# Optimization experiments

Measured on AMD Instinct MI355X. Metric: run time of the kernel, lower is better.

The kernel has to match this reference:

```python
import jax, jax.numpy as jnp
import numpy as np

D_MODEL = 1024
NUM_HEAD = 16
D_HEAD = D_MODEL // NUM_HEAD
NEG_INF = -1e9


def setup_inputs() -> dict:
    key = jax.random.key(0)
    ks = jax.random.split(key, 10)
    B, S = 16, 512
    v = jax.random.normal(ks[0], (B, S, D_MODEL), dtype=jnp.float32)
    lengths = jax.random.randint(ks[1], (B,), 1, S + 1, dtype=jnp.int32)
    scale = 0.02
    Wq = jax.random.normal(ks[2], (D_MODEL, D_MODEL), dtype=jnp.float32) * scale
    bq = jnp.zeros((D_MODEL,), dtype=jnp.float32)
    Wk = jax.random.normal(ks[3], (D_MODEL, D_MODEL), dtype=jnp.float32) * scale
    bk = jnp.zeros((D_MODEL,), dtype=jnp.float32)
    Wv = jax.random.normal(ks[4], (D_MODEL, D_MODEL), dtype=jnp.float32) * scale
    bv = jnp.zeros((D_MODEL,), dtype=jnp.float32)
    Wo = jax.random.normal(ks[5], (D_MODEL, D_MODEL), dtype=jnp.float32) * scale
    bo = jnp.zeros((D_MODEL,), dtype=jnp.float32)
    return {"v": v, "lengths": lengths, "Wq": Wq, "bq": bq, "Wk": Wk,
            "bk": bk, "Wv": Wv, "bv": bv, "Wo": Wo, "bo": bo}


def reference(v, lengths, Wq, bq, Wk, bk, Wv, bv, Wo, bo):
    B, S, D = v.shape
    H, Dh = NUM_HEAD, D_HEAD
    # key-padding mask: True where key position j is valid (j < lengths[b])
    valid = jnp.arange(S)[None, :] < lengths[:, None]          # [B, S]
    # project q, k, v and split heads -> [B, H, S, Dh]
    def split_heads(x):
        return x.reshape(B, S, H, Dh).transpose(0, 2, 1, 3)
    q = split_heads(v @ Wq + bq)
    k = split_heads(v @ Wk + bk)
    val = split_heads(v @ Wv + bv)
    scores = jnp.einsum('bhqd,bhkd->bhqk', q, k) / jnp.sqrt(jnp.float32(Dh))
    scores = jnp.where(valid[:, None, None, :], scores, NEG_INF)  # mask padded keys
    attn = jax.nn.softmax(scores, axis=-1)
    out = jnp.einsum('bhqk,bhkd->bhqd', attn, val)              # [B, H, S, Dh]
    out = out.transpose(0, 2, 1, 3).reshape(B, S, D)
    return out @ Wo + bo
```

## Files before the change

### kernel.cpp

```cpp
#include <hip/hip_runtime.h>
#include <hip/hip_bf16.h>

typedef unsigned short u16;
typedef __attribute__((ext_vector_type(8))) short short8;
typedef __attribute__((ext_vector_type(4))) float f32x4;

#define B_SZ 16
#define S_SZ 512
#define D_SZ 1024
#define H_SZ 16
#define DH_SZ 64
#define M_SZ (B_SZ * S_SZ)
#define EXPSCALE 0.18033688f

__device__ __forceinline__ void gload_lds16(const void* g, void* l) {
  __builtin_amdgcn_global_load_lds(
      (const __attribute__((address_space(1))) unsigned int*)g,
      (__attribute__((address_space(3))) unsigned int*)l,
      16, 0, 0);
}

__global__ __launch_bounds__(256) void prep(
    const float* __restrict__ v, u16* __restrict__ vB,
    const float* __restrict__ W0, const float* __restrict__ W1,
    const float* __restrict__ W2, const float* __restrict__ W3,
    u16* __restrict__ T0, u16* __restrict__ T1,
    u16* __restrict__ T2, u16* __restrict__ T3) {
  __shared__ float tile[32][33];
  const int bid = blockIdx.x;
  if (bid < 8192) {
    int i = bid * 256 + threadIdx.x;
    const float4 f = *(const float4*)&v[(size_t)i * 4];
    ushort4 o; __hip_bfloat16 h;
    h = __float2bfloat16(f.x); o.x = *(u16*)&h;
    h = __float2bfloat16(f.y); o.y = *(u16*)&h;
    h = __float2bfloat16(f.z); o.z = *(u16*)&h;
    h = __float2bfloat16(f.w); o.w = *(u16*)&h;
    *(ushort4*)&vB[(size_t)i * 4] = o;
    return;
  }
  const int tb = bid - 8192;
  const int z = tb >> 10, rem = tb & 1023;
  const int by = rem >> 5, bx = rem & 31;
  const float* W; u16* T;
  switch (z) {
    case 0: W = W0; T = T0; break;
    case 1: W = W1; T = T1; break;
    case 2: W = W2; T = T2; break;
    default: W = W3; T = T3; break;
  }
  int tx = threadIdx.x & 31, ty = threadIdx.x >> 5;
  int x = bx * 32 + tx;
#pragma unroll
  for (int i = 0; i < 32; i += 8)
    tile[ty + i][tx] = W[(size_t)(by * 32 + ty + i) * 1024 + x];
  __syncthreads();
  int x2 = by * 32 + tx;
#pragma unroll
  for (int i = 0; i < 32; i += 8) {
    __hip_bfloat16 h = __float2bfloat16(tile[tx][ty + i]);
    T[(size_t)(bx * 32 + ty + i) * 1024 + x2] = *(u16*)&h;
  }
}

struct G8 {
  const u16* A; const u16* Bt;
  u16* As; u16* Bs;
  int m0, n0;
  int wave, c, quad, r7, wm, wn;
  int srow, slc8;
};

#define AS_T (128 * 64)
#define BS_T (256 * 64)

__device__ __forceinline__ void stage_a(const G8& g, int buf, int kt, int i) {
  const int grp = g.wave * 2 + i;
  gload_lds16(&g.A[(size_t)(g.m0 + grp * 8 + g.srow) * 1024 + kt * 64 + g.slc8],
              g.As + buf * AS_T + grp * 512);
}
__device__ __forceinline__ void stage_b(const G8& g, int buf, int kt, int i) {
  const int grp = g.wave * 4 + i;
  gload_lds16(&g.Bt[(size_t)(g.n0 + grp * 8 + g.srow) * 1024 + kt * 64 + g.slc8],
              g.Bs + buf * BS_T + grp * 512);
}

template<bool ST, int VM>
__device__ __forceinline__ void tile_step(const G8& g, int cur, int stg, int kt2,
                                          f32x4 acc[4][4]) {
  const u16* ab = g.As + cur * AS_T;
  const u16* bb = g.Bs + cur * BS_T;
  short8 af[4], bf[4];

  {
    const int pc = (g.quad ^ g.r7) * 8;
#pragma unroll
    for (int i = 0; i < 4; ++i) {
      af[i] = *(const short8*)&ab[(g.wm + i * 16 + g.c) * 64 + pc];
      bf[i] = *(const short8*)&bb[(g.wn + i * 16 + g.c) * 64 + pc];
    }
    if constexpr (ST) {
      stage_a(g, stg, kt2, 0);
      stage_a(g, stg, kt2, 1);
      stage_b(g, stg, kt2, 0);
    }
    __builtin_amdgcn_s_barrier();
    __builtin_amdgcn_s_setprio(1);
#pragma unroll
    for (int mi = 0; mi < 4; ++mi)
#pragma unroll
      for (int ni = 0; ni < 4; ++ni)
        acc[mi][ni] = __builtin_amdgcn_mfma_f32_16x16x32_bf16(
            af[mi], bf[ni], acc[mi][ni], 0, 0, 0);
    __builtin_amdgcn_s_setprio(0);
    __builtin_amdgcn_s_barrier();
  }

  {
    const int pc = ((4 + g.quad) ^ g.r7) * 8;
#pragma unroll
    for (int i = 0; i < 4; ++i) {
      af[i] = *(const short8*)&ab[(g.wm + i * 16 + g.c) * 64 + pc];
      bf[i] = *(const short8*)&bb[(g.wn + i * 16 + g.c) * 64 + pc];
    }
    if constexpr (ST) {
      stage_b(g, stg, kt2, 1);
      stage_b(g, stg, kt2, 2);
      stage_b(g, stg, kt2, 3);
    }
    __builtin_amdgcn_s_barrier();
    __builtin_amdgcn_s_setprio(1);
#pragma unroll
    for (int mi = 0; mi < 4; ++mi)
#pragma unroll
      for (int ni = 0; ni < 4; ++ni)
        acc[mi][ni] = __builtin_amdgcn_mfma_f32_16x16x32_bf16(
            af[mi], bf[ni], acc[mi][ni], 0, 0, 0);
    __builtin_amdgcn_s_setprio(0);
    if constexpr (VM == 6) {
      asm volatile("s_waitcnt vmcnt(6)" ::: "memory");
      __builtin_amdgcn_s_barrier();
    } else if constexpr (VM == 0) {
      asm volatile("s_waitcnt vmcnt(0)" ::: "memory");
      __builtin_amdgcn_s_barrier();
    }
  }
}

__device__ __forceinline__ void gemm_core8(
    const u16* __restrict__ A, const u16* __restrict__ Bt,
    u16* AsB, u16* BsB, int m0, int n0, f32x4 acc[4][4]) {
  const int tid = threadIdx.x;
  const int lane = tid & 63;
  G8 g;
  g.A = A; g.Bt = Bt; g.As = AsB; g.Bs = BsB;
  g.m0 = m0; g.n0 = n0;
  g.wave = tid >> 6;
  g.c = lane & 15; g.quad = lane >> 4; g.r7 = g.c & 7;
  g.wm = (g.wave >> 2) * 64;
  g.wn = (g.wave & 3) * 64;
  g.srow = lane >> 3;
  g.slc8 = ((lane & 7) ^ g.srow) * 8;

  stage_a(g, 0, 0, 0); stage_a(g, 0, 0, 1);
  stage_b(g, 0, 0, 0); stage_b(g, 0, 0, 1); stage_b(g, 0, 0, 2); stage_b(g, 0, 0, 3);
  stage_a(g, 1, 1, 0); stage_a(g, 1, 1, 1);
  stage_b(g, 1, 1, 0); stage_b(g, 1, 1, 1); stage_b(g, 1, 1, 2); stage_b(g, 1, 1, 3);
  asm volatile("s_waitcnt vmcnt(6)" ::: "memory");
  __builtin_amdgcn_s_barrier();

  int cur = 0, stg = 2;
#pragma unroll 1
  for (int t = 0; t < 14; ++t) {
    tile_step<true, 6>(g, cur, stg, t + 2, acc);
    cur = (cur == 2) ? 0 : cur + 1;
    stg = (stg == 2) ? 0 : stg + 1;
  }
  tile_step<false, 0>(g, cur, 0, 0, acc);
  tile_step<false, -1>(g, 0, 0, 0, acc);
}

template<int Z>
__global__ __launch_bounds__(512, 2) void gemm_split(
    const u16* __restrict__ A, const u16* __restrict__ Bt,
    const float* __restrict__ bias, u16* __restrict__ Out) {
  __shared__ u16 As[3][AS_T];
  __shared__ u16 Bs[3][BS_T];
  const int m0 = blockIdx.x * 128, n0 = blockIdx.y * 256;

  f32x4 acc[4][4];
#pragma unroll
  for (int i = 0; i < 4; ++i)
#pragma unroll
    for (int j = 0; j < 4; ++j) acc[i][j] = f32x4{0.f, 0.f, 0.f, 0.f};

  gemm_core8(A, Bt, &As[0][0], &Bs[0][0], m0, n0, acc);

  const int lane = threadIdx.x & 63, wave = threadIdx.x >> 6;
  const int wm = (wave >> 2) * 64, wn = (wave & 3) * 64;
  const int c = lane & 15, quad = lane >> 4;
#pragma unroll
  for (int ni = 0; ni < 4; ++ni) {
    int n = n0 + wn + ni * 16 + c;
    float bval = bias[n];
#pragma unroll
    for (int mi = 0; mi < 4; ++mi) {
      int mb = m0 + wm + mi * 16 + quad * 4;
      if constexpr (Z == 2) {
        int bb = mb >> 9, s = mb & 511, hh = n >> 6, d = n & 63;
        ushort4 st;
        __hip_bfloat16 h0 = __float2bfloat16(acc[mi][ni][0] + bval); st.x = *(u16*)&h0;
        __hip_bfloat16 h1 = __float2bfloat16(acc[mi][ni][1] + bval); st.y = *(u16*)&h1;
        __hip_bfloat16 h2 = __float2bfloat16(acc[mi][ni][2] + bval); st.z = *(u16*)&h2;
        __hip_bfloat16 h3 = __float2bfloat16(acc[mi][ni][3] + bval); st.w = *(u16*)&h3;
        *(ushort4*)&Out[(((size_t)(bb * 16 + hh) * 64 + d) << 9) + s] = st;
      } else {
#pragma unroll
        for (int r = 0; r < 4; ++r) {
          int m = mb + r;
          float val = acc[mi][ni][r] + bval;
          __hip_bfloat16 hb = __float2bfloat16(val);
          if constexpr (Z == 0) {
            Out[(size_t)m * 1024 + n] = *(u16*)&hb;
          } else {
            int bb = m >> 9, s = m & 511, hh = n >> 6, d = n & 63;
            Out[(((size_t)(bb * 16 + hh) * 512 + s) << 6) + d] = *(u16*)&hb;
          }
        }
      }
    }
  }
}

__global__ __launch_bounds__(512, 2) void gemm_out(
    const u16* __restrict__ A, const u16* __restrict__ Bt,
    const float* __restrict__ bias, float* __restrict__ Cf) {
  __shared__ u16 As[3][AS_T];
  __shared__ u16 Bs[3][BS_T];
  const int m0 = blockIdx.x * 128, n0 = blockIdx.y * 256;

  f32x4 acc[4][4];
#pragma unroll
  for (int i = 0; i < 4; ++i)
#pragma unroll
    for (int j = 0; j < 4; ++j) acc[i][j] = f32x4{0.f, 0.f, 0.f, 0.f};

  gemm_core8(A, Bt, &As[0][0], &Bs[0][0], m0, n0, acc);

  const int lane = threadIdx.x & 63, wave = threadIdx.x >> 6;
  const int wm = (wave >> 2) * 64, wn = (wave & 3) * 64;
  const int c = lane & 15, quad = lane >> 4;
#pragma unroll
  for (int ni = 0; ni < 4; ++ni) {
    int n = n0 + wn + ni * 16 + c;
    float bval = bias[n];
#pragma unroll
    for (int mi = 0; mi < 4; ++mi) {
#pragma unroll
      for (int r = 0; r < 4; ++r) {
        int m = m0 + wm + mi * 16 + quad * 4 + r;
        Cf[(size_t)m * 1024 + n] = acc[mi][ni][r] + bval;
      }
    }
  }
}

__global__ __launch_bounds__(256) void attn_v6(
    const u16* __restrict__ Q, const u16* __restrict__ Kt,
    const u16* __restrict__ Vt, const int* __restrict__ lengths,
    u16* __restrict__ O) {
  const int qc = blockIdx.x, h = blockIdx.y, b = blockIdx.z;
  const int t = threadIdx.x;
  const int lane = t & 63, wave = t >> 6;
  const int c = lane & 15, quad = lane >> 4;
  const int kb = quad * 8;
  const int len = lengths[b];
  const int q0 = qc * 128 + wave * 32;

  __shared__ __align__(16) u16 Ks[64 * 64];
  __shared__ __align__(16) u16 Vs[64 * 64];
  __shared__ __align__(16) u16 Pt[4][32 * 72];

  const size_t bBase = (size_t)b * (S_SZ * D_SZ);
  const size_t hBase = ((size_t)(b * H_SZ + h)) * (S_SZ * DH_SZ);

  short8 aq[2][2];
#pragma unroll
  for (int qt = 0; qt < 2; ++qt) {
    aq[qt][0] = *(const short8*)&Q[bBase + (size_t)(q0 + qt * 16 + c) * 1024 + h * 64 + kb];
    aq[qt][1] = *(const short8*)&Q[bBase + (size_t)(q0 + qt * 16 + c) * 1024 + h * 64 + 32 + kb];
  }

  const int srow = lane >> 3;
  const int slc = (lane & 7) ^ srow;

  float rs[2] = {0.f, 0.f};
  f32x4 o[2][4];
#pragma unroll
  for (int qt = 0; qt < 2; ++qt)
#pragma unroll
    for (int i = 0; i < 4; ++i) o[qt][i] = f32x4{0.f, 0.f, 0.f, 0.f};

  const int kmax = (len + 63) & ~63;
  for (int k0 = 0; k0 < kmax; k0 += 64) {
    __syncthreads();
#pragma unroll
    for (int g = 0; g < 2; ++g) {
      const int rb = (wave * 2 + g) * 8;
      gload_lds16(&Kt[hBase + (size_t)(k0 + rb + srow) * 64 + slc * 8],
                  &Ks[(wave * 2 + g) * 512]);
      gload_lds16(&Vt[hBase + (size_t)(rb + srow) * 512 + k0 + slc * 8],
                  &Vs[(wave * 2 + g) * 512]);
    }
    __syncthreads();

#pragma unroll
    for (int sub = 0; sub < 4; ++sub) {
      const int row = sub * 16 + c;
      short8 bk0 = *(const short8*)&Ks[row * 64 + ((quad ^ (c & 7))) * 8];
      short8 bk1 = *(const short8*)&Ks[row * 64 + (((4 + quad) ^ (c & 7))) * 8];
      const int keyb = k0 + sub * 16 + quad * 4;
#pragma unroll
      for (int qt = 0; qt < 2; ++qt) {
        f32x4 s = {0.f, 0.f, 0.f, 0.f};
        s = __builtin_amdgcn_mfma_f32_16x16x32_bf16(bk0, aq[qt][0], s, 0, 0, 0);
        s = __builtin_amdgcn_mfma_f32_16x16x32_bf16(bk1, aq[qt][1], s, 0, 0, 0);
        ushort4 st;
        float p0 = (keyb + 0) < len ? exp2f(s[0] * EXPSCALE) : 0.f;
        float p1 = (keyb + 1) < len ? exp2f(s[1] * EXPSCALE) : 0.f;
        float p2 = (keyb + 2) < len ? exp2f(s[2] * EXPSCALE) : 0.f;
        float p3 = (keyb + 3) < len ? exp2f(s[3] * EXPSCALE) : 0.f;
        __hip_bfloat16 h0 = __float2bfloat16(p0); st.x = *(u16*)&h0;
        __hip_bfloat16 h1 = __float2bfloat16(p1); st.y = *(u16*)&h1;
        __hip_bfloat16 h2 = __float2bfloat16(p2); st.z = *(u16*)&h2;
        __hip_bfloat16 h3 = __float2bfloat16(p3); st.w = *(u16*)&h3;
        rs[qt] += __bfloat162float(h0) + __bfloat162float(h1) +
                  __bfloat162float(h2) + __bfloat162float(h3);
        *(ushort4*)&Pt[wave][(qt * 16 + c) * 72 + sub * 16 + quad * 4] = st;
      }
    }
#pragma unroll
    for (int ksub = 0; ksub < 2; ++ksub) {
      const short8 pa0 = *(const short8*)&Pt[wave][(c) * 72 + ksub * 32 + kb];
      const short8 pa1 = *(const short8*)&Pt[wave][(16 + c) * 72 + ksub * 32 + kb];
#pragma unroll
      for (int dt = 0; dt < 4; ++dt) {
        const int vrow = dt * 16 + c;
        short8 vb = *(const short8*)&Vs[vrow * 64 + (((ksub * 4 + quad) ^ (c & 7))) * 8];
        o[0][dt] = __builtin_amdgcn_mfma_f32_16x16x32_bf16(pa0, vb, o[0][dt], 0, 0, 0);
        o[1][dt] = __builtin_amdgcn_mfma_f32_16x16x32_bf16(pa1, vb, o[1][dt], 0, 0, 0);
      }
    }
  }

#pragma unroll
  for (int qt = 0; qt < 2; ++qt) {
    rs[qt] += __shfl_xor(rs[qt], 16, 64);
    rs[qt] += __shfl_xor(rs[qt], 32, 64);
  }

#pragma unroll
  for (int qt = 0; qt < 2; ++qt) {
    float lq[4];
#pragma unroll
    for (int r = 0; r < 4; ++r) lq[r] = __shfl(rs[qt], quad * 4 + r, 16);
#pragma unroll
    for (int dt = 0; dt < 4; ++dt) {
#pragma unroll
      for (int r = 0; r < 4; ++r) {
        int s = q0 + qt * 16 + quad * 4 + r;
        float val = o[qt][dt][r] / lq[r];
        __hip_bfloat16 ob = __float2bfloat16(val);
        O[bBase + (size_t)s * 1024 + h * 64 + dt * 16 + c] = *(u16*)&ob;
      }
    }
  }
}

extern "C" void kernel_launch(void* const* d_in, const int* in_sizes, int n_in,
                              void* d_out, int out_size, void* d_ws, size_t ws_size,
                              hipStream_t stream) {
  const float* v  = (const float*)d_in[0];
  const int* lengths = (const int*)d_in[1];
  const float* Wq = (const float*)d_in[2];
  const float* bq = (const float*)d_in[3];
  const float* Wk = (const float*)d_in[4];
  const float* bk = (const float*)d_in[5];
  const float* Wv = (const float*)d_in[6];
  const float* bv = (const float*)d_in[7];
  const float* Wo = (const float*)d_in[8];
  const float* bo = (const float*)d_in[9];

  char* ws = (char*)d_ws;
  const size_t TSZ = (size_t)M_SZ * D_SZ * 2;
  const size_t WSZ = (size_t)1 << 21;
  u16* vB  = (u16*)(ws);
  u16* AO  = vB;
  u16* WqT = (u16*)(ws + TSZ + 0 * WSZ);
  u16* WkT = (u16*)(ws + TSZ + 1 * WSZ);
  u16* WvT = (u16*)(ws + TSZ + 2 * WSZ);
  u16* WoT = (u16*)(ws + TSZ + 3 * WSZ);
  u16* Qb  = (u16*)(ws + TSZ + 4 * WSZ + 0 * TSZ);
  u16* Kt  = (u16*)(ws + TSZ + 4 * WSZ + 1 * TSZ);
  u16* Vt  = (u16*)(ws + TSZ + 4 * WSZ + 2 * TSZ);

  prep<<<dim3(8192 + 4096), 256, 0, stream>>>(v, vB, Wq, Wk, Wv, Wo, WqT, WkT, WvT, WoT);

  gemm_split<0><<<dim3(64, 4), 512, 0, stream>>>(vB, WqT, bq, Qb);
  gemm_split<1><<<dim3(64, 4), 512, 0, stream>>>(vB, WkT, bk, Kt);
  gemm_split<2><<<dim3(64, 4), 512, 0, stream>>>(vB, WvT, bv, Vt);

  attn_v6<<<dim3(4, 16, 16), 256, 0, stream>>>(Qb, Kt, Vt, lengths, AO);

  gemm_out<<<dim3(64, 4), 512, 0, stream>>>(AO, WoT, bo, (float*)d_out);
}
```

Before: 224.7 us.

## Fold softmax scale into Q projection and compute row sums via MFMA

Folds the exp2 softmax scale into the Q projection epilogue, which removes a multiply per score in attention. It splits the masking into a fast path for full key tiles and a masked path for the tail tile. The row-sum of probabilities is now computed by an extra MFMA against a ones vector instead of scalar adds and cross-lane shuffles, and the final division becomes a reciprocal multiply. The trade-off is extra MFMA work and a rounding change from scaling Q before the bf16 conversion.

```diff
diff --git a/kernel.cpp b/kernel.cpp
--- a/kernel.cpp
+++ b/kernel.cpp
@@ -219,6 +219,7 @@
         for (int r = 0; r < 4; ++r) {
           int m = mb + r;
           float val = acc[mi][ni][r] + bval;
+          if constexpr (Z == 0) val *= EXPSCALE;
           __hip_bfloat16 hb = __float2bfloat16(val);
           if constexpr (Z == 0) {
             Out[(size_t)m * 1024 + n] = *(u16*)&hb;
@@ -265,7 +266,7 @@
   }
 }
 
-__global__ __launch_bounds__(256) void attn_v6(
+__global__ __launch_bounds__(256) void attn_v8(
     const u16* __restrict__ Q, const u16* __restrict__ Kt,
     const u16* __restrict__ Vt, const int* __restrict__ lengths,
     u16* __restrict__ O) {
@@ -291,15 +292,20 @@
     aq[qt][1] = *(const short8*)&Q[bBase + (size_t)(q0 + qt * 16 + c) * 1024 + h * 64 + 32 + kb];
   }
 
+  const short ONE = (short)0x3F80;
+  const short8 ones = {ONE, ONE, ONE, ONE, ONE, ONE, ONE, ONE};
+
   const int srow = lane >> 3;
   const int slc = (lane & 7) ^ srow;
 
-  float rs[2] = {0.f, 0.f};
   f32x4 o[2][4];
-#pragma unroll
-  for (int qt = 0; qt < 2; ++qt)
+  f32x4 osum[2];
+#pragma unroll
+  for (int qt = 0; qt < 2; ++qt) {
+    osum[qt] = f32x4{0.f, 0.f, 0.f, 0.f};
 #pragma unroll
     for (int i = 0; i < 4; ++i) o[qt][i] = f32x4{0.f, 0.f, 0.f, 0.f};
+  }
 
   const int kmax = (len + 63) & ~63;
   for (int k0 = 0; k0 < kmax; k0 += 64) {
@@ -314,6 +320,8 @@
     }
     __syncthreads();
 
+    const bool full = (k0 + 64 <= len);
+
 #pragma unroll
     for (int sub = 0; sub < 4; ++sub) {
       const int row = sub * 16 + c;
@@ -325,17 +333,21 @@
         f32x4 s = {0.f, 0.f, 0.f, 0.f};
         s = __builtin_amdgcn_mfma_f32_16x16x32_bf16(bk0, aq[qt][0], s, 0, 0, 0);
         s = __builtin_amdgcn_mfma_f32_16x16x32_bf16(bk1, aq[qt][1], s, 0, 0, 0);
+        float p0, p1, p2, p3;
+        if (full) {
+          p0 = exp2f(s[0]); p1 = exp2f(s[1]);
+          p2 = exp2f(s[2]); p3 = exp2f(s[3]);
+        } else {
+          p0 = (keyb + 0) < len ? exp2f(s[0]) : 0.f;
+          p1 = (keyb + 1) < len ? exp2f(s[1]) : 0.f;
+          p2 = (keyb + 2) < len ? exp2f(s[2]) : 0.f;
+          p3 = (keyb + 3) < len ? exp2f(s[3]) : 0.f;
+        }
         ushort4 st;
-        float p0 = (keyb + 0) < len ? exp2f(s[0] * EXPSCALE) : 0.f;
-        float p1 = (keyb + 1) < len ? exp2f(s[1] * EXPSCALE) : 0.f;
-        float p2 = (keyb + 2) < len ? exp2f(s[2] * EXPSCALE) : 0.f;
-        float p3 = (keyb + 3) < len ? exp2f(s[3] * EXPSCALE) : 0.f;
         __hip_bfloat16 h0 = __float2bfloat16(p0); st.x = *(u16*)&h0;
         __hip_bfloat16 h1 = __float2bfloat16(p1); st.y = *(u16*)&h1;
         __hip_bfloat16 h2 = __float2bfloat16(p2); st.z = *(u16*)&h2;
         __hip_bfloat16 h3 = __float2bfloat16(p3); st.w = *(u16*)&h3;
-        rs[qt] += __bfloat162float(h0) + __bfloat162float(h1) +
-                  __bfloat162float(h2) + __bfloat162float(h3);
         *(ushort4*)&Pt[wave][(qt * 16 + c) * 72 + sub * 16 + quad * 4] = st;
       }
     }
@@ -343,6 +355,8 @@
     for (int ksub = 0; ksub < 2; ++ksub) {
       const short8 pa0 = *(const short8*)&Pt[wave][(c) * 72 + ksub * 32 + kb];
       const short8 pa1 = *(const short8*)&Pt[wave][(16 + c) * 72 + ksub * 32 + kb];
+      osum[0] = __builtin_amdgcn_mfma_f32_16x16x32_bf16(pa0, ones, osum[0], 0, 0, 0);
+      osum[1] = __builtin_amdgcn_mfma_f32_16x16x32_bf16(pa1, ones, osum[1], 0, 0, 0);
 #pragma unroll
       for (int dt = 0; dt < 4; ++dt) {
         const int vrow = dt * 16 + c;
@@ -355,21 +369,15 @@
 
 #pragma unroll
   for (int qt = 0; qt < 2; ++qt) {
-    rs[qt] += __shfl_xor(rs[qt], 16, 64);
-    rs[qt] += __shfl_xor(rs[qt], 32, 64);
-  }
-
-#pragma unroll
-  for (int qt = 0; qt < 2; ++qt) {
-    float lq[4];
-#pragma unroll
-    for (int r = 0; r < 4; ++r) lq[r] = __shfl(rs[qt], quad * 4 + r, 16);
+    float inv[4];
+#pragma unroll
+    for (int r = 0; r < 4; ++r) inv[r] = 1.0f / osum[qt][r];
 #pragma unroll
     for (int dt = 0; dt < 4; ++dt) {
 #pragma unroll
       for (int r = 0; r < 4; ++r) {
         int s = q0 + qt * 16 + quad * 4 + r;
-        float val = o[qt][dt][r] / lq[r];
+        float val = o[qt][dt][r] * inv[r];
         __hip_bfloat16 ob = __float2bfloat16(val);
         O[bBase + (size_t)s * 1024 + h * 64 + dt * 16 + c] = *(u16*)&ob;
       }
@@ -410,7 +418,7 @@
   gemm_split<1><<<dim3(64, 4), 512, 0, stream>>>(vB, WkT, bk, Kt);
   gemm_split<2><<<dim3(64, 4), 512, 0, stream>>>(vB, WvT, bv, Vt);
 
-  attn_v6<<<dim3(4, 16, 16), 256, 0, stream>>>(Qb, Kt, Vt, lengths, AO);
+  attn_v8<<<dim3(4, 16, 16), 256, 0, stream>>>(Qb, Kt, Vt, lengths, AO);
 
   gemm_out<<<dim3(64, 4), 512, 0, stream>>>(AO, WoT, bo, (float*)d_out);
 }
```

After: 219.7 us. 1.02x faster.
